# Performance work log

Hardware: AMD Instinct MI355X
Metric: run time of the kernel (lower is better)

## Reference

```python
import jax, jax.numpy as jnp
import numpy as np

N = 50000
E = 800000
EL = 100000
IN_CH = 33
HID = 64
OUT = 128
NTYPES = 311
EMB = 16
COMB = IN_CH - 1 + EMB  # 48


def setup_inputs() -> dict:
    key = jax.random.key(0)
    ks = jax.random.split(key, 24)
    # x: col 0 = node type (integer-valued float), rest = float features
    types = jax.random.randint(ks[0], (N, 1), 0, NTYPES).astype(jnp.float32)
    feats = jax.random.normal(ks[1], (N, IN_CH - 1), dtype=jnp.float32)
    x = jnp.concatenate([types, feats], axis=1)
    edge_index = jax.random.randint(ks[2], (2, E), 0, N, dtype=jnp.int32)
    edge_label_index = jax.random.randint(ks[3], (2, EL), 0, N, dtype=jnp.int32)
    s = 0.05
    inp = {
        'x': x, 'edge_index': edge_index, 'edge_label_index': edge_label_index,
        'emb': jax.random.normal(ks[4], (NTYPES, EMB)) * s,
        'W1': jax.random.normal(ks[5], (COMB, 4 * HID)) * s,
        'a_src1': jax.random.normal(ks[6], (4, HID)) * s,
        'a_dst1': jax.random.normal(ks[7], (4, HID)) * s,
        'b1': jnp.zeros((4 * HID,)),
        'W2': jax.random.normal(ks[8], (4 * HID, 2 * 2 * HID)) * s,
        'a_src2': jax.random.normal(ks[9], (2, 2 * HID)) * s,
        'a_dst2': jax.random.normal(ks[10], (2, 2 * HID)) * s,
        'b2': jnp.zeros((2 * 2 * HID,)),
        'W3': jax.random.normal(ks[11], (4 * HID, OUT)) * s,
        'a_src3': jax.random.normal(ks[12], (1, OUT)) * s,
        'a_dst3': jax.random.normal(ks[13], (1, OUT)) * s,
        'b3': jnp.zeros((OUT,)),
        'Wl1': jax.random.normal(ks[14], (2 * OUT, HID)) * s,
        'bl1': jnp.zeros((HID,)),
        'Wl2': jax.random.normal(ks[15], (HID, 1)) * s,
        'bl2': jnp.zeros((1,)),
        'trans_bias': jax.random.normal(ks[16], (NTYPES, NTYPES)) * s,
    }
    return inp


def _gat(h_in, src, dst, W, a_src, a_dst, b, heads, d_out):
    # linear transform, per-head split
    h = (h_in @ W).reshape(N, heads, d_out)                      # [N,H,D]
    al_s = jnp.einsum('nhd,hd->nh', h, a_src)                    # [N,H]
    al_d = jnp.einsum('nhd,hd->nh', h, a_dst)
    logits = jax.nn.leaky_relu(al_s[src] + al_d[dst], 0.2)       # [E,H]
    m = jax.ops.segment_max(logits, dst, num_segments=N)
    m = jnp.where(jnp.isfinite(m), m, 0.0)
    e = jnp.exp(logits - m[dst])
    denom = jax.ops.segment_sum(e, dst, num_segments=N)
    alpha = e / (denom[dst] + 1e-16)                             # [E,H]
    msg = h[src] * alpha[:, :, None]                             # [E,H,D]
    out = jax.ops.segment_sum(msg, dst, num_segments=N)          # [N,H,D]
    return out.reshape(N, heads * d_out) + b


def reference(x, edge_index, edge_label_index, emb, W1, a_src1, a_dst1, b1,
              W2, a_src2, a_dst2, b2, W3, a_src3, a_dst3, b3,
              Wl1, bl1, Wl2, bl2, trans_bias):
    node_types = x[:, 0].astype(jnp.int32)
    x_comb = jnp.concatenate([emb[node_types], x[:, 1:]], axis=1)  # [N,48]
    # add self loops (PyG GATConv default)
    loops = jnp.arange(N, dtype=edge_index.dtype)
    ei = jnp.concatenate([edge_index, jnp.stack([loops, loops])], axis=1)
    src, dst = ei[0], ei[1]
    z = jax.nn.elu(_gat(x_comb, src, dst, W1, a_src1, a_dst1, b1, 4, HID))
    z = jax.nn.elu(_gat(z, src, dst, W2, a_src2, a_dst2, b2, 2, 2 * HID))
    z = _gat(z, src, dst, W3, a_src3, a_dst3, b3, 1, OUT)
    # decode
    ls, ld = edge_label_index[0], edge_label_index[1]
    ef = jnp.concatenate([z[ls], z[ld]], axis=1)                  # [EL,2*OUT]
    h = jax.nn.relu(ef @ Wl1 + bl1)
    base = h @ Wl2 + bl2                                          # [EL,1]
    bias = trans_bias[node_types[ls], node_types[ld]][:, None]
    return base + bias
```

## Files before the change

kernel.cpp:

```cpp
#include <hip/hip_runtime.h>
#include <hip/hip_bf16.h>

#define NN 50000
#define EE 800000
#define ELN 100000
#define ETOT (EE + NN)
#define NT 311

#define NBUCK ((NN + 127) >> 7)
#define BCAP 3072
#define CHUNK 8192

typedef _Float16 f16;
typedef f16 f16x8 __attribute__((ext_vector_type(8)));
typedef f16 f16x4 __attribute__((ext_vector_type(4)));
typedef f16 f16x2 __attribute__((ext_vector_type(2)));
typedef float f32x4 __attribute__((ext_vector_type(4)));

__device__ __forceinline__ float edge_alpha(float l)
{
    l = l > 0.f ? l : 0.2f * l;
    return __expf(fminf(l, 80.f));
}

__global__ __launch_bounds__(256) void k_prepatt(const float* __restrict__ x,
                                                 const float* __restrict__ emb,
                                                 const float* __restrict__ a1ps,
                                                 const float* __restrict__ a1pd,
                                                 f16* __restrict__ xc,
                                                 int* __restrict__ ntypes,
                                                 float* __restrict__ als,
                                                 float* __restrict__ ald)
{
    int gid = blockIdx.x * 256 + threadIdx.x;
    int n = gid >> 6, lane = gid & 63;
    if (n >= NN) return;
    int tpe = (int)x[(size_t)n * 33];
    tpe = tpe < 0 ? 0 : (tpe > NT - 1 ? NT - 1 : tpe);
    if (lane == 0) ntypes[n] = tpe;
    float v;
    if (lane < 16)      v = emb[tpe * 16 + lane];
    else if (lane < 48) v = x[(size_t)n * 33 + 1 + (lane - 16)];
    else                v = 0.f;
    f16 hv = (f16)v;
    xc[(size_t)n * 64 + lane] = hv;
    float xv = (float)hv;
    float ps[4], pd[4];
    #pragma unroll
    for (int h = 0; h < 4; ++h) {
        ps[h] = xv * a1ps[h * 64 + lane];
        pd[h] = xv * a1pd[h * 64 + lane];
    }
    #pragma unroll
    for (int off = 32; off > 0; off >>= 1) {
        #pragma unroll
        for (int h = 0; h < 4; ++h) {
            ps[h] += __shfl_xor(ps[h], off, 64);
            pd[h] += __shfl_xor(pd[h], off, 64);
        }
    }
    if (lane == 0) {
        #pragma unroll
        for (int h = 0; h < 4; ++h) {
            als[n * 4 + h] = ps[h];
            ald[n * 4 + h] = pd[h];
        }
    }
}

__global__ __launch_bounds__(256) void k_cvtall(const float* __restrict__ W1,
                                                const float* __restrict__ W2,
                                                const float* __restrict__ W3,
                                                const float* __restrict__ Wl1,
                                                f16* __restrict__ Wt1,
                                                f16* __restrict__ Wt2,
                                                f16* __restrict__ Wt3,
                                                f16* __restrict__ Wtl)
{
    int idx = blockIdx.x * 256 + threadIdx.x;
    if (idx < 16384) {
        int h = idx >> 12, c = (idx >> 6) & 63, k = idx & 63;
        Wt1[idx] = (k < 48) ? (f16)W1[(size_t)k * 256 + h * 64 + c] : (f16)0.f;
    } else if (idx < 81920) {
        int i = idx - 16384;
        int c = i >> 8, k = i & 255;
        Wt2[i] = (f16)W2[(size_t)k * 256 + c];
    } else if (idx < 114688) {
        int i = idx - 81920;
        int c = i >> 8, k = i & 255;
        Wt3[i] = (f16)W3[(size_t)k * 128 + c];
    } else if (idx < 131072) {
        int i = idx - 114688;
        int c = i >> 8, k = i & 255;
        Wtl[i] = (f16)Wl1[(size_t)k * 64 + c];
    }
}

__global__ __launch_bounds__(256) void k_pre1(const float* __restrict__ W1,
                                              const float* __restrict__ as1,
                                              const float* __restrict__ ad1,
                                              float* __restrict__ a1ps,
                                              float* __restrict__ a1pd)
{
    int t = threadIdx.x;
    int h = t >> 6, k = t & 63;
    float ss = 0.f, sd = 0.f;
    if (k < 48) {
        for (int d = 0; d < 64; ++d) {
            float w = W1[(size_t)k * 256 + h * 64 + d];
            ss += w * as1[h * 64 + d];
            sd += w * ad1[h * 64 + d];
        }
    }
    a1ps[t] = ss;
    a1pd[t] = sd;
}

__global__ __launch_bounds__(256) void k_bucket(const int* __restrict__ ei,
                                                int* __restrict__ bcur,
                                                int2* __restrict__ bbuf)
{
    __shared__ int hist[NBUCK];
    __shared__ int gbase[NBUCK];
    const int t = threadIdx.x;
    for (int i = t; i < NBUCK; i += 256) hist[i] = 0;
    __syncthreads();
    const int e0 = blockIdx.x * CHUNK;
    const int eend = min(e0 + CHUNK, ETOT);
    for (int e = e0 + t; e < eend; e += 256) {
        int dst = (e < EE) ? ei[EE + e] : (e - EE);
        atomicAdd(&hist[dst >> 7], 1);
    }
    __syncthreads();
    for (int i = t; i < NBUCK; i += 256) {
        int c = hist[i];
        gbase[i] = c ? atomicAdd(&bcur[i], c) : 0;
        hist[i] = 0;
    }
    __syncthreads();
    for (int e = e0 + t; e < eend; e += 256) {
        int src, dst;
        if (e < EE) { src = ei[e]; dst = ei[EE + e]; }
        else        { src = e - EE; dst = src; }
        int b = dst >> 7;
        int pos = gbase[b] + atomicAdd(&hist[b], 1);
        if (pos < BCAP)
            bbuf[(size_t)b * BCAP + pos] = make_int2(src, dst);
    }
}

__global__ __launch_bounds__(512) void k_bscan(const int* __restrict__ bcur,
                                               int* __restrict__ boff)
{
    __shared__ int s[512];
    int t = threadIdx.x;
    int v = (t < NBUCK) ? min(bcur[t], BCAP) : 0;
    s[t] = v;
    __syncthreads();
    #pragma unroll
    for (int off = 1; off < 512; off <<= 1) {
        int u = (t >= off) ? s[t - off] : 0;
        __syncthreads();
        s[t] += u;
        __syncthreads();
    }
    if (t < NBUCK) boff[t] = s[t] - v;
    if (t == NBUCK - 1) boff[NBUCK] = s[t];
}

__global__ __launch_bounds__(256) void k_csrb(const int* __restrict__ bcur,
                                              const int* __restrict__ boff,
                                              const int2* __restrict__ bbuf,
                                              int* __restrict__ rowptr,
                                              int* __restrict__ csr)
{
    __shared__ int nh[128];
    __shared__ int loff[128];
    __shared__ int ncur[128];
    __shared__ int ssrc[BCAP];
    const int b = blockIdx.x;
    const int t = threadIdx.x;
    const int n0 = b << 7;
    const int cnt = min(bcur[b], BCAP);
    const int base = boff[b];
    const size_t bb = (size_t)b * BCAP;
    if (t < 128) { nh[t] = 0; ncur[t] = 0; }
    __syncthreads();
    for (int i = t; i < cnt; i += 256)
        atomicAdd(&nh[bbuf[bb + i].y - n0], 1);
    __syncthreads();
    int myc = (t < 128) ? nh[t] : 0;
    #pragma unroll
    for (int off = 1; off < 128; off <<= 1) {
        int u = (t >= off && t < 128) ? nh[t - off] : 0;
        __syncthreads();
        if (t < 128) nh[t] += u;
        __syncthreads();
    }
    if (t < 128) {
        int ex = nh[t] - myc;
        loff[t] = ex;
        int n = n0 + t;
        if (n < NN) rowptr[n] = base + ex;
    }
    __syncthreads();
    for (int i = t; i < cnt; i += 256) {
        int2 p = bbuf[bb + i];
        int ln = p.y - n0;
        int pos = loff[ln] + atomicAdd(&ncur[ln], 1);
        ssrc[pos] = p.x;
    }
    __syncthreads();
    for (int i = t; i < cnt; i += 256)
        csr[base + i] = ssrc[i];
    if (b == 0 && t == 0) rowptr[NN] = boff[NBUCK];
}

template<int K, int CN, int H>
__global__ __launch_bounds__(256) void k_gemmh(const f16* __restrict__ A,
                                               const f16* __restrict__ Wt,
                                               f16* __restrict__ O,
                                               int nrows,
                                               const float* __restrict__ asrc,
                                               const float* __restrict__ adst,
                                               float* __restrict__ als,
                                               float* __restrict__ ald)
{
    constexpr int LDA = 40;
    __shared__ f16 As[64 * LDA];
    __shared__ f16 Bs[64 * LDA];
    const int t = threadIdx.x;
    const int w = t >> 6;
    const int lane = t & 63;
    const int m = lane & 15;
    const int quad = lane >> 4;
    const int row0 = blockIdx.x * 64;
    const int col0 = blockIdx.y * 64;
    const int r_st = t >> 2;
    const int seg  = (t & 3) * 8;
    f32x4 acc[4] = {{0.f,0.f,0.f,0.f},{0.f,0.f,0.f,0.f},{0.f,0.f,0.f,0.f},{0.f,0.f,0.f,0.f}};
    for (int k0 = 0; k0 < K; k0 += 32) {
        int gr = row0 + r_st;
        f16x8 av = {0,0,0,0,0,0,0,0};
        if (gr < nrows) av = *(const f16x8*)&A[(size_t)gr * K + k0 + seg];
        *(f16x8*)&As[r_st * LDA + seg] = av;
        f16x8 bv = *(const f16x8*)&Wt[(size_t)(col0 + r_st) * K + k0 + seg];
        *(f16x8*)&Bs[r_st * LDA + seg] = bv;
        __syncthreads();
        f16x8 af = *(const f16x8*)&As[(w * 16 + m) * LDA + quad * 8];
        #pragma unroll
        for (int g = 0; g < 4; ++g) {
            f16x8 bf = *(const f16x8*)&Bs[(g * 16 + m) * LDA + quad * 8];
            acc[g] = __builtin_amdgcn_mfma_f32_16x16x32_f16(af, bf, acc[g], 0, 0, 0);
        }
        __syncthreads();
    }
    #pragma unroll
    for (int g = 0; g < 4; ++g) {
        #pragma unroll
        for (int reg = 0; reg < 4; ++reg) {
            int gr = row0 + w * 16 + quad * 4 + reg;
            int gc = col0 + g * 16 + m;
            if (gr < nrows) O[(size_t)gr * CN + gc] = (f16)acc[g][reg];
        }
    }
    if constexpr (H > 0) {
        constexpr int D = CN / H;
        const int head = col0 / D;
        float ps[4] = {}, pd[4] = {};
        #pragma unroll
        for (int g = 0; g < 4; ++g) {
            int col = col0 + g * 16 + m;
            float a_s = asrc[col], a_d = adst[col];
            #pragma unroll
            for (int reg = 0; reg < 4; ++reg) {
                ps[reg] += acc[g][reg] * a_s;
                pd[reg] += acc[g][reg] * a_d;
            }
        }
        #pragma unroll
        for (int off = 1; off < 16; off <<= 1) {
            #pragma unroll
            for (int reg = 0; reg < 4; ++reg) {
                ps[reg] += __shfl_xor(ps[reg], off, 64);
                pd[reg] += __shfl_xor(pd[reg], off, 64);
            }
        }
        if (m == 0) {
            #pragma unroll
            for (int reg = 0; reg < 4; ++reg) {
                int gr = row0 + w * 16 + quad * 4 + reg;
                if (gr < nrows) {
                    atomicAdd(&als[gr * H + head], ps[reg]);
                    atomicAdd(&ald[gr * H + head], pd[reg]);
                }
            }
        }
    }
}

__global__ __launch_bounds__(256) void k_gemm1h(const f16* __restrict__ A,
                                                const f16* __restrict__ Wt1,
                                                const float* __restrict__ bias,
                                                f16* __restrict__ O,
                                                int nrows)
{
    constexpr int LDA = 40;
    __shared__ f16 As[64 * LDA];
    __shared__ f16 Bs[64 * LDA];
    const int t = threadIdx.x;
    const int w = t >> 6;
    const int lane = t & 63;
    const int m = lane & 15;
    const int quad = lane >> 4;
    const int row0 = blockIdx.x * 64;
    const int head = blockIdx.y;
    const int r_st = t >> 2;
    const int seg  = (t & 3) * 8;
    f32x4 acc[4] = {{0.f,0.f,0.f,0.f},{0.f,0.f,0.f,0.f},{0.f,0.f,0.f,0.f},{0.f,0.f,0.f,0.f}};
    for (int k0 = 0; k0 < 64; k0 += 32) {
        int gr = row0 + r_st;
        f16x8 av = {0,0,0,0,0,0,0,0};
        if (gr < nrows) av = *(const f16x8*)&A[(size_t)gr * 256 + head * 64 + k0 + seg];
        *(f16x8*)&As[r_st * LDA + seg] = av;
        f16x8 bv = *(const f16x8*)&Wt1[(size_t)head * 4096 + (size_t)r_st * 64 + k0 + seg];
        *(f16x8*)&Bs[r_st * LDA + seg] = bv;
        __syncthreads();
        f16x8 af = *(const f16x8*)&As[(w * 16 + m) * LDA + quad * 8];
        #pragma unroll
        for (int g = 0; g < 4; ++g) {
            f16x8 bf = *(const f16x8*)&Bs[(g * 16 + m) * LDA + quad * 8];
            acc[g] = __builtin_amdgcn_mfma_f32_16x16x32_f16(af, bf, acc[g], 0, 0, 0);
        }
        __syncthreads();
    }
    #pragma unroll
    for (int g = 0; g < 4; ++g) {
        #pragma unroll
        for (int reg = 0; reg < 4; ++reg) {
            int gr = row0 + w * 16 + quad * 4 + reg;
            int col = head * 64 + g * 16 + m;
            if (gr < nrows) {
                float v = acc[g][reg] + bias[col];
                v = v > 0.f ? v : (__expf(v) - 1.f);
                O[(size_t)gr * 256 + col] = (f16)v;
            }
        }
    }
}

__global__ __launch_bounds__(256) void k_aggx(const int* __restrict__ rowptr,
                                              const int* __restrict__ csr,
                                              const float* __restrict__ als,
                                              const float* __restrict__ ald,
                                              const f16* __restrict__ xc,
                                              f16* __restrict__ xagg)
{
    int gid = blockIdx.x * 256 + threadIdx.x;
    int n = gid >> 6, lane = gid & 63;
    if (n >= NN) return;
    int p  = lane >> 5;
    int cb = (lane & 31) * 2;
    int r0 = rowptr[n], r1 = rowptr[n + 1];
    float4 dl = *(const float4*)&ald[(size_t)n * 4];
    float a0[2] = {}, a1[2] = {}, a2[2] = {}, a3[2] = {};
    float d0 = 0.f, d1 = 0.f, d2 = 0.f, d3 = 0.f;
    int i = r0;
    for (; i + 8 <= r1; i += 8) {
        int s[4]; float4 A[4]; f16x2 xv[4]; float4 e[4];
        #pragma unroll
        for (int k = 0; k < 4; ++k) s[k] = csr[i + 2 * k + p];
        #pragma unroll
        for (int k = 0; k < 4; ++k) xv[k] = *(const f16x2*)&xc[(size_t)s[k] * 64 + cb];
        #pragma unroll
        for (int k = 0; k < 4; ++k) A[k] = *(const float4*)&als[(size_t)s[k] * 4];
        #pragma unroll
        for (int k = 0; k < 4; ++k) {
            e[k].x = edge_alpha(A[k].x + dl.x);
            e[k].y = edge_alpha(A[k].y + dl.y);
            e[k].z = edge_alpha(A[k].z + dl.z);
            e[k].w = edge_alpha(A[k].w + dl.w);
        }
        #pragma unroll
        for (int k = 0; k < 4; ++k) {
            #pragma unroll
            for (int j = 0; j < 2; ++j) {
                float v0 = (float)xv[k][j];
                a0[j] += e[k].x * v0;
                a1[j] += e[k].y * v0;
                a2[j] += e[k].z * v0;
                a3[j] += e[k].w * v0;
            }
            d0 += e[k].x; d1 += e[k].y; d2 += e[k].z; d3 += e[k].w;
        }
    }
    for (; i < r1; i += 2) {
        int ii = i + p;
        bool v = ii < r1;
        int s0 = csr[v ? ii : r0];
        float4 A0 = *(const float4*)&als[(size_t)s0 * 4];
        float4 e0;
        e0.x = v ? edge_alpha(A0.x + dl.x) : 0.f;
        e0.y = v ? edge_alpha(A0.y + dl.y) : 0.f;
        e0.z = v ? edge_alpha(A0.z + dl.z) : 0.f;
        e0.w = v ? edge_alpha(A0.w + dl.w) : 0.f;
        f16x2 x0 = *(const f16x2*)&xc[(size_t)s0 * 64 + cb];
        #pragma unroll
        for (int j = 0; j < 2; ++j) {
            float v0 = (float)x0[j];
            a0[j] += e0.x * v0; a1[j] += e0.y * v0;
            a2[j] += e0.z * v0; a3[j] += e0.w * v0;
        }
        d0 += e0.x; d1 += e0.y; d2 += e0.z; d3 += e0.w;
    }
    #pragma unroll
    for (int j = 0; j < 2; ++j) {
        a0[j] += __shfl_xor(a0[j], 32, 64);
        a1[j] += __shfl_xor(a1[j], 32, 64);
        a2[j] += __shfl_xor(a2[j], 32, 64);
        a3[j] += __shfl_xor(a3[j], 32, 64);
    }
    d0 += __shfl_xor(d0, 32, 64);
    d1 += __shfl_xor(d1, 32, 64);
    d2 += __shfl_xor(d2, 32, 64);
    d3 += __shfl_xor(d3, 32, 64);
    if (p == 0) {
        float i0 = 1.f / d0, i1 = 1.f / d1, i2 = 1.f / d2, i3 = 1.f / d3;
        size_t base = (size_t)n * 256 + cb;
        f16x2 o0 = {(f16)(a0[0] * i0), (f16)(a0[1] * i0)};
        f16x2 o1 = {(f16)(a1[0] * i1), (f16)(a1[1] * i1)};
        f16x2 o2 = {(f16)(a2[0] * i2), (f16)(a2[1] * i2)};
        f16x2 o3 = {(f16)(a3[0] * i3), (f16)(a3[1] * i3)};
        *(f16x2*)&xagg[base]       = o0;
        *(f16x2*)&xagg[base + 64]  = o1;
        *(f16x2*)&xagg[base + 128] = o2;
        *(f16x2*)&xagg[base + 192] = o3;
    }
}

__global__ __launch_bounds__(256) void k_agg2f(const int* __restrict__ rowptr,
                                               const int* __restrict__ csr,
                                               const float* __restrict__ als,
                                               const float* __restrict__ ald,
                                               const f16* __restrict__ h,
                                               const float* __restrict__ bias,
                                               f16* __restrict__ z)
{
    int gid = blockIdx.x * 256 + threadIdx.x;
    int n = gid >> 6, lane = gid & 63;
    if (n >= NN) return;
    int p  = lane >> 5;
    int cb = (lane & 31) * 8;
    int head = (lane & 31) >> 4;
    int r0 = rowptr[n], r1 = rowptr[n + 1];
    float dd = ald[(size_t)n * 2 + head];
    float a[8] = {};
    float den = 0.f;
    int i = r0;
    for (; i + 16 <= r1; i += 16) {
        int s[8]; f16x8 hv[8]; float e[8];
        #pragma unroll
        for (int k = 0; k < 8; ++k) s[k] = csr[i + 2 * k + p];
        #pragma unroll
        for (int k = 0; k < 8; ++k) hv[k] = *(const f16x8*)&h[(size_t)s[k] * 256 + cb];
        #pragma unroll
        for (int k = 0; k < 8; ++k) e[k] = edge_alpha(als[(size_t)s[k] * 2 + head] + dd);
        #pragma unroll
        for (int k = 0; k < 8; ++k) {
            den += e[k];
            #pragma unroll
            for (int j = 0; j < 8; ++j) a[j] += e[k] * (float)hv[k][j];
        }
    }
    for (; i + 8 <= r1; i += 8) {
        int s[4]; f16x8 hv[4]; float e[4];
        #pragma unroll
        for (int k = 0; k < 4; ++k) s[k] = csr[i + 2 * k + p];
        #pragma unroll
        for (int k = 0; k < 4; ++k) hv[k] = *(const f16x8*)&h[(size_t)s[k] * 256 + cb];
        #pragma unroll
        for (int k = 0; k < 4; ++k) e[k] = edge_alpha(als[(size_t)s[k] * 2 + head] + dd);
        #pragma unroll
        for (int k = 0; k < 4; ++k) {
            den += e[k];
            #pragma unroll
            for (int j = 0; j < 8; ++j) a[j] += e[k] * (float)hv[k][j];
        }
    }
    for (; i < r1; i += 2) {
        int ii = i + p;
        bool v = ii < r1;
        int s0 = csr[v ? ii : r0];
        float e0 = v ? edge_alpha(als[(size_t)s0 * 2 + head] + dd) : 0.f;
        f16x8 h0 = *(const f16x8*)&h[(size_t)s0 * 256 + cb];
        #pragma unroll
        for (int j = 0; j < 8; ++j) a[j] += e0 * (float)h0[j];
        den += e0;
    }
    #pragma unroll
    for (int j = 0; j < 8; ++j) a[j] += __shfl_xor(a[j], 32, 64);
    den += __shfl_xor(den, 32, 64);
    if (p == 0) {
        float inv = 1.f / den;
        f16x8 o;
        #pragma unroll
        for (int j = 0; j < 8; ++j) {
            float v = a[j] * inv + bias[cb + j];
            v = v > 0.f ? v : (__expf(v) - 1.f);
            o[j] = (f16)v;
        }
        *(f16x8*)&z[(size_t)n * 256 + cb] = o;
    }
}

__global__ __launch_bounds__(256) void k_agg3(const int* __restrict__ rowptr,
                                              const int* __restrict__ csr,
                                              const float* __restrict__ als,
                                              const float* __restrict__ ald,
                                              const f16* __restrict__ h,
                                              const float* __restrict__ bias,
                                              f16* __restrict__ z)
{
    int gid = blockIdx.x * 256 + threadIdx.x;
    int n = gid >> 6, lane = gid & 63;
    if (n >= NN) return;
    int p  = lane >> 4;
    int cb = (lane & 15) * 8;
    int r0 = rowptr[n], r1 = rowptr[n + 1];
    float dd = ald[n];
    float a[8] = {};
    float den = 0.f;
    int i = r0;
    for (; i + 16 <= r1; i += 16) {
        int s[4]; f16x8 hv[4]; float e[4];
        #pragma unroll
        for (int k = 0; k < 4; ++k) s[k] = csr[i + 4 * k + p];
        #pragma unroll
        for (int k = 0; k < 4; ++k) hv[k] = *(const f16x8*)&h[(size_t)s[k] * 128 + cb];
        #pragma unroll
        for (int k = 0; k < 4; ++k) e[k] = edge_alpha(als[s[k]] + dd);
        #pragma unroll
        for (int k = 0; k < 4; ++k) {
            den += e[k];
            #pragma unroll
            for (int j = 0; j < 8; ++j) a[j] += e[k] * (float)hv[k][j];
        }
    }
    for (; i + 8 <= r1; i += 8) {
        int s[2]; f16x8 hv[2]; float e[2];
        #pragma unroll
        for (int k = 0; k < 2; ++k) s[k] = csr[i + 4 * k + p];
        #pragma unroll
        for (int k = 0; k < 2; ++k) hv[k] = *(const f16x8*)&h[(size_t)s[k] * 128 + cb];
        #pragma unroll
        for (int k = 0; k < 2; ++k) e[k] = edge_alpha(als[s[k]] + dd);
        #pragma unroll
        for (int k = 0; k < 2; ++k) {
            den += e[k];
            #pragma unroll
            for (int j = 0; j < 8; ++j) a[j] += e[k] * (float)hv[k][j];
        }
    }
    for (; i < r1; i += 4) {
        int ii = i + p;
        bool v = ii < r1;
        int s0 = csr[v ? ii : r0];
        float e0 = v ? edge_alpha(als[s0] + dd) : 0.f;
        f16x8 h0 = *(const f16x8*)&h[(size_t)s0 * 128 + cb];
        #pragma unroll
        for (int j = 0; j < 8; ++j) a[j] += e0 * (float)h0[j];
        den += e0;
    }
    #pragma unroll
    for (int j = 0; j < 8; ++j) {
        a[j] += __shfl_xor(a[j], 16, 64);
        a[j] += __shfl_xor(a[j], 32, 64);
    }
    den += __shfl_xor(den, 16, 64);
    den += __shfl_xor(den, 32, 64);
    if (lane < 16) {
        float inv = 1.f / den;
        f16x8 o;
        #pragma unroll
        for (int j = 0; j < 8; ++j)
            o[j] = (f16)(a[j] * inv + bias[cb + j]);
        *(f16x8*)&z[(size_t)n * 128 + cb] = o;
    }
}

#define DLDA 264
__global__ __launch_bounds__(256) void k_decm(const f16* __restrict__ z3,
                                              const int* __restrict__ eli,
                                              const int* __restrict__ ntypes,
                                              const f16* __restrict__ Wtl,
                                              const float* __restrict__ bl1,
                                              const float* __restrict__ Wl2,
                                              const float* __restrict__ bl2,
                                              const float* __restrict__ tb,
                                              float* __restrict__ out)
{
    __shared__ f16 As[64 * DLDA];
    __shared__ int sls[64], sld[64];
    const int t = threadIdx.x;
    const int e0 = blockIdx.x * 64;
    if (t < 64) {
        int e = e0 + t;
        sls[t] = (e < ELN) ? eli[e] : 0;
        sld[t] = (e < ELN) ? eli[ELN + e] : 0;
    }
    __syncthreads();
    {
        int r = t & 63;
        int seg = t >> 6;
        int base = seg * 64;
        int node = (base < 128) ? sls[r] : sld[r];
        int zoff = base & 127;
        #pragma unroll
        for (int j = 0; j < 8; ++j) {
            f16x8 v = *(const f16x8*)&z3[(size_t)node * 128 + zoff + j * 8];
            *(f16x8*)&As[r * DLDA + base + j * 8] = v;
        }
    }
    __syncthreads();
    const int w = t >> 6;
    const int lane = t & 63;
    const int m = lane & 15;
    const int quad = lane >> 4;
    f32x4 acc[4] = {{0.f,0.f,0.f,0.f},{0.f,0.f,0.f,0.f},{0.f,0.f,0.f,0.f},{0.f,0.f,0.f,0.f}};
    for (int k0 = 0; k0 < 256; k0 += 32) {
        f16x8 af = *(const f16x8*)&As[(w * 16 + m) * DLDA + k0 + quad * 8];
        #pragma unroll
        for (int g = 0; g < 4; ++g) {
            f16x8 bf = *(const f16x8*)&Wtl[(size_t)(g * 16 + m) * 256 + k0 + quad * 8];
            acc[g] = __builtin_amdgcn_mfma_f32_16x16x32_f16(af, bf, acc[g], 0, 0, 0);
        }
    }
    float s[4] = {0.f, 0.f, 0.f, 0.f};
    #pragma unroll
    for (int g = 0; g < 4; ++g) {
        int col = g * 16 + m;
        float b = bl1[col], wv = Wl2[col];
        #pragma unroll
        for (int reg = 0; reg < 4; ++reg) {
            float hv = fmaxf(acc[g][reg] + b, 0.f);
            s[reg] += hv * wv;
        }
    }
    #pragma unroll
    for (int off = 1; off < 16; off <<= 1) {
        #pragma unroll
        for (int reg = 0; reg < 4; ++reg) s[reg] += __shfl_xor(s[reg], off, 64);
    }
    if (m == 0) {
        float b2v = bl2[0];
        #pragma unroll
        for (int reg = 0; reg < 4; ++reg) {
            int r = w * 16 + quad * 4 + reg;
            int e = e0 + r;
            if (e < ELN) {
                out[e] = s[reg] + b2v +
                         tb[(size_t)ntypes[sls[r]] * NT + ntypes[sld[r]]];
            }
        }
    }
}

extern "C" void kernel_launch(void* const* d_in, const int* in_sizes, int n_in,
                              void* d_out, int out_size, void* d_ws, size_t ws_size,
                              hipStream_t stream)
{
    const float* x   = (const float*)d_in[0];
    const int*   ei  = (const int*)d_in[1];
    const int*   eli = (const int*)d_in[2];
    const float* emb = (const float*)d_in[3];
    const float* W1  = (const float*)d_in[4];
    const float* as1 = (const float*)d_in[5];
    const float* ad1 = (const float*)d_in[6];
    const float* b1  = (const float*)d_in[7];
    const float* W2  = (const float*)d_in[8];
    const float* as2 = (const float*)d_in[9];
    const float* ad2 = (const float*)d_in[10];
    const float* b2  = (const float*)d_in[11];
    const float* W3  = (const float*)d_in[12];
    const float* as3 = (const float*)d_in[13];
    const float* ad3 = (const float*)d_in[14];
    const float* b3  = (const float*)d_in[15];
    const float* Wl1 = (const float*)d_in[16];
    const float* bl1 = (const float*)d_in[17];
    const float* Wl2 = (const float*)d_in[18];
    const float* bl2 = (const float*)d_in[19];
    const float* tb  = (const float*)d_in[20];
    float* out = (float*)d_out;

    char* ws = (char*)d_ws;
    size_t off = 0;
    auto alloc = [&](size_t bytes) { size_t o = off; off = (off + bytes + 255) & ~(size_t)255; return o; };
    int*   ntypes = (int*)  (ws + alloc((size_t)NN * 4));
    f16*   xc16   = (f16*)  (ws + alloc((size_t)NN * 64 * 2));
    int*   rowptr = (int*)  (ws + alloc((size_t)(NN + 1) * 4));
    int*   csr    = (int*)  (ws + alloc((size_t)ETOT * 4));
    int*   bcur   = (int*)  (ws + alloc((size_t)(NBUCK + 1) * 4));
    int*   boff   = (int*)  (ws + alloc((size_t)(NBUCK + 1) * 4));
    float* scores = (float*)(ws + alloc((size_t)NN * 14 * 4));
    float* als1 = scores;
    float* ald1 = scores + (size_t)NN * 4;
    float* als2 = scores + (size_t)NN * 8;
    float* ald2 = scores + (size_t)NN * 10;
    float* als3 = scores + (size_t)NN * 12;
    float* ald3 = scores + (size_t)NN * 13;
    int2*  bbuf   = (int2*) (ws + alloc((size_t)NBUCK * BCAP * 8));
    f16*   h16    = (f16*)  (ws + alloc((size_t)NN * 256 * 2));
    f16*   z16    = (f16*)  (ws + alloc((size_t)NN * 256 * 2));
    f16*   Wt1    = (f16*)  (ws + alloc((size_t)4 * 64 * 64 * 2));
    f16*   Wt2    = (f16*)  (ws + alloc((size_t)256 * 256 * 2));
    f16*   Wt3    = (f16*)  (ws + alloc((size_t)128 * 256 * 2));
    f16*   Wtl    = (f16*)  (ws + alloc((size_t)64 * 256 * 2));
    float* a1ps   = (float*)(ws + alloc(256 * 4));
    float* a1pd   = (float*)(ws + alloc(256 * 4));

    hipMemsetAsync(bcur, 0, (size_t)(NBUCK + 1) * 4, stream);
    hipMemsetAsync(als2, 0, (size_t)NN * 6 * 4, stream);

    const int RB   = (NN + 63) / 64;
    const int gW1  = (NN + 3) / 4;

    k_pre1<<<1, 256, 0, stream>>>(W1, as1, ad1, a1ps, a1pd);
    k_prepatt<<<gW1, 256, 0, stream>>>(x, emb, a1ps, a1pd, xc16, ntypes, als1, ald1);
    k_cvtall<<<(131072 + 255) / 256, 256, 0, stream>>>(W1, W2, W3, Wl1, Wt1, Wt2, Wt3, Wtl);

    k_bucket<<<(ETOT + CHUNK - 1) / CHUNK, 256, 0, stream>>>(ei, bcur, bbuf);
    k_bscan <<<1, 512, 0, stream>>>(bcur, boff);
    k_csrb  <<<NBUCK, 256, 0, stream>>>(bcur, boff, bbuf, rowptr, csr);

    k_aggx<<<gW1, 256, 0, stream>>>(rowptr, csr, als1, ald1, xc16, h16 );
    k_gemm1h<<<dim3(RB, 4), 256, 0, stream>>>(h16 , Wt1, b1, z16, NN);

    k_gemmh<256, 256, 2><<<dim3(RB, 4), 256, 0, stream>>>(z16, Wt2, h16, NN, as2, ad2, als2, ald2);
    k_agg2f<<<gW1, 256, 0, stream>>>(rowptr, csr, als2, ald2, h16, b2, z16);

    k_gemmh<256, 128, 1><<<dim3(RB, 2), 256, 0, stream>>>(z16, Wt3, h16, NN, as3, ad3, als3, ald3);
    k_agg3<<<gW1, 256, 0, stream>>>(rowptr, csr, als3, ald3, h16, b3, z16);

    k_decm<<<(ELN + 63) / 64, 256, 0, stream>>>(z16, eli, ntypes, Wtl, bl1, Wl2, bl2, tb, out);
}
```

Measured before the change: 422.4 us.

## Split aggregation kernels into feature slices mapped across XCDs

The three GAT aggregation kernels now split each node's feature vector into 8 slices. Blocks are interleaved so that consecutive block IDs handle different slices, which under round-robin dispatch places each slice on its own XCD. The intent is for each XCD's L2 to cache only its slice of the gathered source-feature table, improving the gather hit rate. In exchange, the CSR row and attention scalars are read 8 times, each edge's exp is recomputed per slice, gathers are narrower, cross-lane reductions are longer, and nontemporal loads and stores are added.

Measured after the change: 835.9 us. 1.98x slower.

```diff
diff --git a/kernel.cpp b/kernel.cpp
--- a/kernel.cpp
+++ b/kernel.cpp
@@ -10,6 +10,8 @@
 #define NBUCK ((NN + 127) >> 7)
 #define BCAP 3072
 #define CHUNK 8192
+
+#define NXCD 8
 
 typedef _Float16 f16;
 typedef f16 f16x8 __attribute__((ext_vector_type(8)));
@@ -349,81 +351,77 @@
     }
 }
 
-__global__ __launch_bounds__(256) void k_aggx(const int* __restrict__ rowptr,
-                                              const int* __restrict__ csr,
-                                              const float* __restrict__ als,
-                                              const float* __restrict__ ald,
-                                              const f16* __restrict__ xc,
-                                              f16* __restrict__ xagg)
-{
-    int gid = blockIdx.x * 256 + threadIdx.x;
-    int n = gid >> 6, lane = gid & 63;
+
+__global__ __launch_bounds__(256) void k_aggxs(const int* __restrict__ rowptr,
+                                               const int* __restrict__ csr,
+                                               const float* __restrict__ als,
+                                               const float* __restrict__ ald,
+                                               const f16* __restrict__ xc,
+                                               f16* __restrict__ xagg)
+{
+    int b = blockIdx.x;
+    int slice = b & (NXCD - 1);
+    int ng = b >> 3;
+    int t = threadIdx.x;
+    int n = ng * 4 + (t >> 6);
     if (n >= NN) return;
-    int p  = lane >> 5;
-    int cb = (lane & 31) * 2;
+    int lane = t & 63;
+    int p  = lane >> 2;
+    int fl = lane & 3;
+    int cb = slice * 8 + fl * 2;
     int r0 = rowptr[n], r1 = rowptr[n + 1];
     float4 dl = *(const float4*)&ald[(size_t)n * 4];
     float a0[2] = {}, a1[2] = {}, a2[2] = {}, a3[2] = {};
     float d0 = 0.f, d1 = 0.f, d2 = 0.f, d3 = 0.f;
     int i = r0;
-    for (; i + 8 <= r1; i += 8) {
-        int s[4]; float4 A[4]; f16x2 xv[4]; float4 e[4];
-        #pragma unroll
-        for (int k = 0; k < 4; ++k) s[k] = csr[i + 2 * k + p];
-        #pragma unroll
-        for (int k = 0; k < 4; ++k) xv[k] = *(const f16x2*)&xc[(size_t)s[k] * 64 + cb];
-        #pragma unroll
-        for (int k = 0; k < 4; ++k) A[k] = *(const float4*)&als[(size_t)s[k] * 4];
-        #pragma unroll
-        for (int k = 0; k < 4; ++k) {
-            e[k].x = edge_alpha(A[k].x + dl.x);
-            e[k].y = edge_alpha(A[k].y + dl.y);
-            e[k].z = edge_alpha(A[k].z + dl.z);
-            e[k].w = edge_alpha(A[k].w + dl.w);
-        }
-        #pragma unroll
-        for (int k = 0; k < 4; ++k) {
-            #pragma unroll
-            for (int j = 0; j < 2; ++j) {
-                float v0 = (float)xv[k][j];
-                a0[j] += e[k].x * v0;
-                a1[j] += e[k].y * v0;
-                a2[j] += e[k].z * v0;
-                a3[j] += e[k].w * v0;
-            }
-            d0 += e[k].x; d1 += e[k].y; d2 += e[k].z; d3 += e[k].w;
-        }
-    }
-    for (; i < r1; i += 2) {
+    for (; i + 16 <= r1; i += 16) {
+        int s0 = __builtin_nontemporal_load(&csr[i + p]);
+        f16x2 xv = *(const f16x2*)&xc[(size_t)s0 * 64 + cb];
+        float4 A0 = *(const float4*)&als[(size_t)s0 * 4];
+        float ex = edge_alpha(A0.x + dl.x);
+        float ey = edge_alpha(A0.y + dl.y);
+        float ez = edge_alpha(A0.z + dl.z);
+        float ew = edge_alpha(A0.w + dl.w);
+        d0 += ex; d1 += ey; d2 += ez; d3 += ew;
+        #pragma unroll
+        for (int j = 0; j < 2; ++j) {
+            float v0 = (float)xv[j];
+            a0[j] += ex * v0; a1[j] += ey * v0;
+            a2[j] += ez * v0; a3[j] += ew * v0;
+        }
+    }
+    for (; i < r1; i += 16) {
         int ii = i + p;
         bool v = ii < r1;
-        int s0 = csr[v ? ii : r0];
+        int s0 = __builtin_nontemporal_load(&csr[v ? ii : r0]);
+        f16x2 xv = *(const f16x2*)&xc[(size_t)s0 * 64 + cb];
         float4 A0 = *(const float4*)&als[(size_t)s0 * 4];
-        float4 e0;
-        e0.x = v ? edge_alpha(A0.x + dl.x) : 0.f;
-        e0.y = v ? edge_alpha(A0.y + dl.y) : 0.f;
-        e0.z = v ? edge_alpha(A0.z + dl.z) : 0.f;
-        e0.w = v ? edge_alpha(A0.w + dl.w) : 0.f;
-        f16x2 x0 = *(const f16x2*)&xc[(size_t)s0 * 64 + cb];
+        float ex = v ? edge_alpha(A0.x + dl.x) : 0.f;
+        float ey = v ? edge_alpha(A0.y + dl.y) : 0.f;
+        float ez = v ? edge_alpha(A0.z + dl.z) : 0.f;
+        float ew = v ? edge_alpha(A0.w + dl.w) : 0.f;
+        d0 += ex; d1 += ey; d2 += ez; d3 += ew;
         #pragma unroll
         for (int j = 0; j < 2; ++j) {
-            float v0 = (float)x0[j];
-            a0[j] += e0.x * v0; a1[j] += e0.y * v0;
-            a2[j] += e0.z * v0; a3[j] += e0.w * v0;
-        }
-        d0 += e0.x; d1 += e0.y; d2 += e0.z; d3 += e0.w;
-    }
-    #pragma unroll
-    for (int j = 0; j < 2; ++j) {
-        a0[j] += __shfl_xor(a0[j], 32, 64);
-        a1[j] += __shfl_xor(a1[j], 32, 64);
-        a2[j] += __shfl_xor(a2[j], 32, 64);
-        a3[j] += __shfl_xor(a3[j], 32, 64);
-    }
-    d0 += __shfl_xor(d0, 32, 64);
-    d1 += __shfl_xor(d1, 32, 64);
-    d2 += __shfl_xor(d2, 32, 64);
-    d3 += __shfl_xor(d3, 32, 64);
+            float v0 = (float)xv[j];
+            a0[j] += ex * v0; a1[j] += ey * v0;
+            a2[j] += ez * v0; a3[j] += ew * v0;
+        }
+    }
+    #pragma unroll
+    for (int off = 4; off < 64; off <<= 1) {
+        #pragma unroll
+        for (int j = 0; j < 2; ++j) {
+            a0[j] += __shfl_xor(a0[j], off, 64);
+            a1[j] += __shfl_xor(a1[j], off, 64);
+            a2[j] += __shfl_xor(a2[j], off, 64);
+            a3[j] += __shfl_xor(a3[j], off, 64);
+        }
+        d0 += __shfl_xor(d0, off, 64);
+        d1 += __shfl_xor(d1, off, 64);
+        d2 += __shfl_xor(d2, off, 64);
+        d3 += __shfl_xor(d3, off, 64);
+    }
     if (p == 0) {
         float i0 = 1.f / d0, i1 = 1.f / d1, i2 = 1.f / d2, i3 = 1.f / d3;
         size_t base = (size_t)n * 256 + cb;
@@ -431,14 +429,14 @@
         f16x2 o1 = {(f16)(a1[0] * i1), (f16)(a1[1] * i1)};
         f16x2 o2 = {(f16)(a2[0] * i2), (f16)(a2[1] * i2)};
         f16x2 o3 = {(f16)(a3[0] * i3), (f16)(a3[1] * i3)};
-        *(f16x2*)&xagg[base]       = o0;
-        *(f16x2*)&xagg[base + 64]  = o1;
-        *(f16x2*)&xagg[base + 128] = o2;
-        *(f16x2*)&xagg[base + 192] = o3;
-    }
-}
-
-__global__ __launch_bounds__(256) void k_agg2f(const int* __restrict__ rowptr,
+        __builtin_nontemporal_store(o0, (f16x2*)&xagg[base]);
+        __builtin_nontemporal_store(o1, (f16x2*)&xagg[base + 64]);
+        __builtin_nontemporal_store(o2, (f16x2*)&xagg[base + 128]);
+        __builtin_nontemporal_store(o3, (f16x2*)&xagg[base + 192]);
+    }
+}
+
+__global__ __launch_bounds__(256) void k_agg2s(const int* __restrict__ rowptr,
                                                const int* __restrict__ csr,
                                                const float* __restrict__ als,
                                                const float* __restrict__ ald,
@@ -446,145 +444,117 @@
                                                const float* __restrict__ bias,
                                                f16* __restrict__ z)
 {
-    int gid = blockIdx.x * 256 + threadIdx.x;
-    int n = gid >> 6, lane = gid & 63;
+    int b = blockIdx.x;
+    int slice = b & (NXCD - 1);
+    int ng = b >> 3;
+    int t = threadIdx.x;
+    int n = ng * 4 + (t >> 6);
     if (n >= NN) return;
-    int p  = lane >> 5;
-    int cb = (lane & 31) * 8;
-    int head = (lane & 31) >> 4;
+    int lane = t & 63;
+    int p  = lane >> 3;
+    int fl = lane & 7;
+    int cb = slice * 32 + fl * 4;
+    int head = slice >> 2;
     int r0 = rowptr[n], r1 = rowptr[n + 1];
     float dd = ald[(size_t)n * 2 + head];
-    float a[8] = {};
+    float a[4] = {};
     float den = 0.f;
     int i = r0;
     for (; i + 16 <= r1; i += 16) {
-        int s[8]; f16x8 hv[8]; float e[8];
-        #pragma unroll
-        for (int k = 0; k < 8; ++k) s[k] = csr[i + 2 * k + p];
-        #pragma unroll
-        for (int k = 0; k < 8; ++k) hv[k] = *(const f16x8*)&h[(size_t)s[k] * 256 + cb];
-        #pragma unroll
-        for (int k = 0; k < 8; ++k) e[k] = edge_alpha(als[(size_t)s[k] * 2 + head] + dd);
-        #pragma unroll
-        for (int k = 0; k < 8; ++k) {
-            den += e[k];
-            #pragma unroll
-            for (int j = 0; j < 8; ++j) a[j] += e[k] * (float)hv[k][j];
-        }
-    }
-    for (; i + 8 <= r1; i += 8) {
-        int s[4]; f16x8 hv[4]; float e[4];
-        #pragma unroll
-        for (int k = 0; k < 4; ++k) s[k] = csr[i + 2 * k + p];
-        #pragma unroll
-        for (int k = 0; k < 4; ++k) hv[k] = *(const f16x8*)&h[(size_t)s[k] * 256 + cb];
-        #pragma unroll
-        for (int k = 0; k < 4; ++k) e[k] = edge_alpha(als[(size_t)s[k] * 2 + head] + dd);
-        #pragma unroll
-        for (int k = 0; k < 4; ++k) {
-            den += e[k];
-            #pragma unroll
-            for (int j = 0; j < 8; ++j) a[j] += e[k] * (float)hv[k][j];
-        }
-    }
-    for (; i < r1; i += 2) {
+        int s0 = __builtin_nontemporal_load(&csr[i + p]);
+        int s1 = __builtin_nontemporal_load(&csr[i + 8 + p]);
+        f16x4 h0 = *(const f16x4*)&h[(size_t)s0 * 256 + cb];
+        f16x4 h1 = *(const f16x4*)&h[(size_t)s1 * 256 + cb];
+        float e0 = edge_alpha(als[(size_t)s0 * 2 + head] + dd);
+        float e1 = edge_alpha(als[(size_t)s1 * 2 + head] + dd);
+        den += e0 + e1;
+        #pragma unroll
+        for (int j = 0; j < 4; ++j)
+            a[j] += e0 * (float)h0[j] + e1 * (float)h1[j];
+    }
+    for (; i < r1; i += 8) {
         int ii = i + p;
         bool v = ii < r1;
-        int s0 = csr[v ? ii : r0];
+        int s0 = __builtin_nontemporal_load(&csr[v ? ii : r0]);
+        f16x4 h0 = *(const f16x4*)&h[(size_t)s0 * 256 + cb];
         float e0 = v ? edge_alpha(als[(size_t)s0 * 2 + head] + dd) : 0.f;
-        f16x8 h0 = *(const f16x8*)&h[(size_t)s0 * 256 + cb];
-        #pragma unroll
-        for (int j = 0; j < 8; ++j) a[j] += e0 * (float)h0[j];
         den += e0;
-    }
-    #pragma unroll
-    for (int j = 0; j < 8; ++j) a[j] += __shfl_xor(a[j], 32, 64);
-    den += __shfl_xor(den, 32, 64);
+        #pragma unroll
+        for (int j = 0; j < 4; ++j) a[j] += e0 * (float)h0[j];
+    }
+    #pragma unroll
+    for (int off = 8; off < 64; off <<= 1) {
+        #pragma unroll
+        for (int j = 0; j < 4; ++j) a[j] += __shfl_xor(a[j], off, 64);
+        den += __shfl_xor(den, off, 64);
+    }
     if (p == 0) {
         float inv = 1.f / den;
-        f16x8 o;
-        #pragma unroll
-        for (int j = 0; j < 8; ++j) {
+        f16x4 o;
+        #pragma unroll
+        for (int j = 0; j < 4; ++j) {
             float v = a[j] * inv + bias[cb + j];
             v = v > 0.f ? v : (__expf(v) - 1.f);
             o[j] = (f16)v;
         }
-        *(f16x8*)&z[(size_t)n * 256 + cb] = o;
-    }
-}
-
-__global__ __launch_bounds__(256) void k_agg3(const int* __restrict__ rowptr,
-                                              const int* __restrict__ csr,
-                                              const float* __restrict__ als,
-                                              const float* __restrict__ ald,
-                                              const f16* __restrict__ h,
-                                              const float* __restrict__ bias,
-                                              f16* __restrict__ z)
-{
-    int gid = blockIdx.x * 256 + threadIdx.x;
-    int n = gid >> 6, lane = gid & 63;
+        __builtin_nontemporal_store(o, (f16x4*)&z[(size_t)n * 256 + cb]);
+    }
+}
+
+__global__ __launch_bounds__(256) void k_agg3s(const int* __restrict__ rowptr,
+                                               const int* __restrict__ csr,
+                                               const float* __restrict__ als,
+                                               const float* __restrict__ ald,
+                                               const f16* __restrict__ h,
+                                               const float* __restrict__ bias,
+                                               f16* __restrict__ z)
+{
+    int b = blockIdx.x;
+    int slice = b & (NXCD - 1);
+    int ng = b >> 3;
+    int t = threadIdx.x;
+    int n = ng * 4 + (t >> 6);
     if (n >= NN) return;
-    int p  = lane >> 4;
-    int cb = (lane & 15) * 8;
+    int lane = t & 63;
+    int p  = lane >> 2;
+    int fl = lane & 3;
+    int cb = slice * 16 + fl * 4;
     int r0 = rowptr[n], r1 = rowptr[n + 1];
     float dd = ald[n];
-    float a[8] = {};
+    float a[4] = {};
     float den = 0.f;
     int i = r0;
     for (; i + 16 <= r1; i += 16) {
-        int s[4]; f16x8 hv[4]; float e[4];
-        #pragma unroll
-        for (int k = 0; k < 4; ++k) s[k] = csr[i + 4 * k + p];
-        #pragma unroll
-        for (int k = 0; k < 4; ++k) hv[k] = *(const f16x8*)&h[(size_t)s[k] * 128 + cb];
-        #pragma unroll
-        for (int k = 0; k < 4; ++k) e[k] = edge_alpha(als[s[k]] + dd);
-        #pragma unroll
-        for (int k = 0; k < 4; ++k) {
-            den += e[k];
-            #pragma unroll
-            for (int j = 0; j < 8; ++j) a[j] += e[k] * (float)hv[k][j];
-        }
-    }
-    for (; i + 8 <= r1; i += 8) {
-        int s[2]; f16x8 hv[2]; float e[2];
-        #pragma unroll
-        for (int k = 0; k < 2; ++k) s[k] = csr[i + 4 * k + p];
-        #pragma unroll
-        for (int k = 0; k < 2; ++k) hv[k] = *(const f16x8*)&h[(size_t)s[k] * 128 + cb];
-        #pragma unroll
-        for (int k = 0; k < 2; ++k) e[k] = edge_alpha(als[s[k]] + dd);
-        #pragma unroll
-        for (int k = 0; k < 2; ++k) {
-            den += e[k];
-            #pragma unroll
-            for (int j = 0; j < 8; ++j) a[j] += e[k] * (float)hv[k][j];
-        }
-    }
-    for (; i < r1; i += 4) {
+        int s0 = __builtin_nontemporal_load(&csr[i + p]);
+        f16x4 h0 = *(const f16x4*)&h[(size_t)s0 * 128 + cb];
+        float e0 = edge_alpha(als[s0] + dd);
+        den += e0;
+        #pragma unroll
+        for (int j = 0; j < 4; ++j) a[j] += e0 * (float)h0[j];
+    }
+    for (; i < r1; i += 16) {
         int ii = i + p;
         bool v = ii < r1;
-        int s0 = csr[v ? ii : r0];
+        int s0 = __builtin_nontemporal_load(&csr[v ? ii : r0]);
+        f16x4 h0 = *(const f16x4*)&h[(size_t)s0 * 128 + cb];
         float e0 = v ? edge_alpha(als[s0] + dd) : 0.f;
-        f16x8 h0 = *(const f16x8*)&h[(size_t)s0 * 128 + cb];
-        #pragma unroll
-        for (int j = 0; j < 8; ++j) a[j] += e0 * (float)h0[j];
         den += e0;
-    }
-    #pragma unroll
-    for (int j = 0; j < 8; ++j) {
-        a[j] += __shfl_xor(a[j], 16, 64);
-        a[j] += __shfl_xor(a[j], 32, 64);
-    }
-    den += __shfl_xor(den, 16, 64);
-    den += __shfl_xor(den, 32, 64);
-    if (lane < 16) {
+        #pragma unroll
+        for (int j = 0; j < 4; ++j) a[j] += e0 * (float)h0[j];
+    }
+    #pragma unroll
+    for (int off = 4; off < 64; off <<= 1) {
+        #pragma unroll
+        for (int j = 0; j < 4; ++j) a[j] += __shfl_xor(a[j], off, 64);
+        den += __shfl_xor(den, off, 64);
+    }
+    if (p == 0) {
         float inv = 1.f / den;
-        f16x8 o;
-        #pragma unroll
-        for (int j = 0; j < 8; ++j)
+        f16x4 o;
+        #pragma unroll
+        for (int j = 0; j < 4; ++j)
             o[j] = (f16)(a[j] * inv + bias[cb + j]);
-        *(f16x8*)&z[(size_t)n * 128 + cb] = o;
+        __builtin_nontemporal_store(o, (f16x4*)&z[(size_t)n * 128 + cb]);
     }
 }
 
@@ -723,6 +693,7 @@
 
     const int RB   = (NN + 63) / 64;
     const int gW1  = (NN + 3) / 4;
+    const int gS   = ((NN + 3) / 4) * NXCD;
 
     k_pre1<<<1, 256, 0, stream>>>(W1, as1, ad1, a1ps, a1pd);
     k_prepatt<<<gW1, 256, 0, stream>>>(x, emb, a1ps, a1pd, xc16, ntypes, als1, ald1);
@@ -732,14 +703,14 @@
     k_bscan <<<1, 512, 0, stream>>>(bcur, boff);
     k_csrb  <<<NBUCK, 256, 0, stream>>>(bcur, boff, bbuf, rowptr, csr);
 
-    k_aggx<<<gW1, 256, 0, stream>>>(rowptr, csr, als1, ald1, xc16, h16 );
+    k_aggxs<<<gS, 256, 0, stream>>>(rowptr, csr, als1, ald1, xc16, h16 );
     k_gemm1h<<<dim3(RB, 4), 256, 0, stream>>>(h16 , Wt1, b1, z16, NN);
 
     k_gemmh<256, 256, 2><<<dim3(RB, 4), 256, 0, stream>>>(z16, Wt2, h16, NN, as2, ad2, als2, ald2);
-    k_agg2f<<<gW1, 256, 0, stream>>>(rowptr, csr, als2, ald2, h16, b2, z16);
+    k_agg2s<<<gS, 256, 0, stream>>>(rowptr, csr, als2, ald2, h16, b2, z16);
 
     k_gemmh<256, 128, 1><<<dim3(RB, 2), 256, 0, stream>>>(z16, Wt3, h16, NN, as3, ad3, als3, ald3);
-    k_agg3<<<gW1, 256, 0, stream>>>(rowptr, csr, als3, ald3, h16, b3, z16);
+    k_agg3s<<<gS, 256, 0, stream>>>(rowptr, csr, als3, ald3, h16, b3, z16);
 
     k_decm<<<(ELN + 63) / 64, 256, 0, stream>>>(z16, eli, ntypes, Wtl, bl1, Wl2, bl2, tb, out);
 }
```
